# Kernel optimization log

Hardware: AMD Instinct MI355X
Metric: run time of the kernel (lower is better)

## Reference

```python
import jax, jax.numpy as jnp
import numpy as np

N_NODES = 50000
D_IN = 256      # input_rep
D_HID = 256     # num_neurons
N_EDGES = 1600000
N_SAMPLES = 100000


def setup_inputs() -> dict:
    key = jax.random.key(0)
    ks = jax.random.split(key, 12)
    x_feature = jax.random.normal(ks[0], (N_NODES, D_IN), dtype=jnp.float32)
    edge_index = jax.random.randint(ks[1], (2, N_EDGES), 0, N_NODES, dtype=jnp.int64)
    samples = jax.random.randint(ks[2], (N_SAMPLES, 2), 0, N_NODES, dtype=jnp.int64)
    s1 = 1.0 / np.sqrt(D_IN)
    s2 = 1.0 / np.sqrt(D_HID)
    W1 = jax.random.uniform(ks[3], (D_IN, D_HID), jnp.float32, -s1, s1)
    b1 = jax.random.uniform(ks[4], (D_HID,), jnp.float32, -s1, s1)
    W2 = jax.random.uniform(ks[5], (D_HID, D_HID), jnp.float32, -s2, s2)
    b2 = jax.random.uniform(ks[6], (D_HID,), jnp.float32, -s2, s2)
    lin1_W = jax.random.uniform(ks[7], (D_IN, D_IN), jnp.float32, -s1, s1)
    lin1_b = jax.random.uniform(ks[8], (D_IN,), jnp.float32, -s1, s1)
    lin2_W = jax.random.uniform(ks[9], (D_IN, 2), jnp.float32, -s1, s1)
    lin2_b = jax.random.uniform(ks[10], (2,), jnp.float32, -s1, s1)
    return {"x_feature": x_feature, "edge_index": edge_index, "samples": samples,
            "W1": W1, "b1": b1, "W2": W2, "b2": b2,
            "lin1_W": lin1_W, "lin1_b": lin1_b, "lin2_W": lin2_W, "lin2_b": lin2_b}


def _gnn_layer(x, src, dst, W, b, n_nodes):
    # sum-aggregate neighbor messages, then linear (standard GCN-style layer)
    agg = jax.ops.segment_sum(x[src], dst, num_segments=n_nodes)  # [N, d]
    return agg @ W + b


def reference(x_feature, edge_index, samples, W1, b1, W2, b2, lin1_W, lin1_b, lin2_W, lin2_b):
    src, dst = edge_index[0], edge_index[1]
    n = x_feature.shape[0]
    # GNN stack (note: its output is discarded in the original forward; kept for faithfulness)
    h = jax.nn.relu(_gnn_layer(x_feature, src, dst, W1, b1, n))
    h = jax.nn.relu(_gnn_layer(h, src, dst, W2, b2, n))
    # fused gather + elementwise multiply over sampled pairs (replaces per-edge Python loop)
    z = x_feature[samples[:, 0]] * x_feature[samples[:, 1]]  # [S, D_IN]
    z = jax.nn.relu(z @ lin1_W + lin1_b)
    return z @ lin2_W + lin2_b  # [S, 2]
```

## Files before the change

kernel.cpp:

```cpp
#include <hip/hip_runtime.h>

typedef __attribute__((ext_vector_type(8))) short bf16x8;
typedef __attribute__((ext_vector_type(4))) float f32x4;

__device__ __forceinline__ unsigned int f2bf(float f) {
    union { float f; unsigned int u; } v; v.f = f;
    unsigned int u = v.u;
    u += 0x7FFFu + ((u >> 16) & 1u);
    return u >> 16;
}

__global__ void pack_w_kernel(const float* __restrict__ W, unsigned short* __restrict__ P) {
    int tid = blockIdx.x * blockDim.x + threadIdx.x;
    if (tid >= 8192) return;
    int kt   = tid >> 10;
    int f    = (tid >> 6) & 15;
    int lane = tid & 63;
    int k0  = kt * 32 + (lane >> 4) * 8;
    int col = f * 16 + (lane & 15);
    bf16x8 v;
    #pragma unroll
    for (int j = 0; j < 8; ++j)
        v[j] = (short)f2bf(W[(k0 + j) * 256 + col]);
    ((bf16x8*)P)[tid] = v;
}

__global__ __launch_bounds__(256, 4)
void fused_kernel(const float* __restrict__ x,
                  const int* __restrict__ samples,
                  const unsigned short* __restrict__ Wp,
                  const float* __restrict__ b1,
                  const float* __restrict__ w2,
                  const float* __restrict__ b2,
                  float* __restrict__ out, int S)
{
    __shared__ unsigned short zt[4][16][264];

    const int tid  = threadIdx.x;
    const int lane = tid & 63;
    const int wave = tid >> 6;
    const int row0 = blockIdx.x * 64 + wave * 16;
    const int cl   = lane & 15;
    const int hi   = lane >> 4;

    int sidx;
    {
        int i    = row0 * 2 + (lane & 31);
        int imax = 2 * S - 1;
        sidx = samples[i < imax ? i : imax];
    }

    #pragma unroll
    for (int rr = 0; rr < 16; rr += 2) {
        int a0 = __shfl(sidx, 2 * rr,     64);
        int b0 = __shfl(sidx, 2 * rr + 1, 64);
        int a1 = __shfl(sidx, 2 * rr + 2, 64);
        int b1i= __shfl(sidx, 2 * rr + 3, 64);
        f32x4 va0 = ((const f32x4*)x)[(size_t)a0 * 64 + lane];
        f32x4 vb0 = ((const f32x4*)x)[(size_t)b0 * 64 + lane];
        f32x4 va1 = ((const f32x4*)x)[(size_t)a1 * 64 + lane];
        f32x4 vb1 = ((const f32x4*)x)[(size_t)b1i * 64 + lane];
        uint2 u0, u1;
        u0.x = f2bf(va0[0] * vb0[0]) | (f2bf(va0[1] * vb0[1]) << 16);
        u0.y = f2bf(va0[2] * vb0[2]) | (f2bf(va0[3] * vb0[3]) << 16);
        u1.x = f2bf(va1[0] * vb1[0]) | (f2bf(va1[1] * vb1[1]) << 16);
        u1.y = f2bf(va1[2] * vb1[2]) | (f2bf(va1[3] * vb1[3]) << 16);
        *(uint2*)&zt[wave][rr][lane * 4]     = u0;
        *(uint2*)&zt[wave][rr + 1][lane * 4] = u1;
    }

    float b1r[16];
    #pragma unroll
    for (int f = 0; f < 16; ++f) b1r[f] = b1[f * 16 + cl];

    f32x4 acc[16];
    #pragma unroll
    for (int f = 0; f < 16; ++f) acc[f] = (f32x4){0.f, 0.f, 0.f, 0.f};

    const bf16x8* wg = (const bf16x8*)Wp;
    for (int kt = 0; kt < 8; ++kt) {
        bf16x8 af = *(const bf16x8*)&zt[wave][cl][kt * 32 + hi * 8];
        const bf16x8* wk = wg + (size_t)kt * 1024 + lane;
        #pragma unroll
        for (int f = 0; f < 16; ++f) {
            bf16x8 bfr = wk[f * 64];
            acc[f] = __builtin_amdgcn_mfma_f32_16x16x32_bf16(af, bfr, acc[f], 0, 0, 0);
        }
    }

    float p0[4] = {0.f, 0.f, 0.f, 0.f};
    float p1[4] = {0.f, 0.f, 0.f, 0.f};
    #pragma unroll
    for (int f = 0; f < 16; ++f) {
        int c = f * 16 + cl;
        float2 lw = ((const float2*)w2)[c];
        #pragma unroll
        for (int q = 0; q < 4; ++q) {
            float h = fmaxf(acc[f][q] + b1r[f], 0.f);
            p0[q] += h * lw.x;
            p1[q] += h * lw.y;
        }
    }
    #pragma unroll
    for (int m = 1; m < 16; m <<= 1) {
        #pragma unroll
        for (int q = 0; q < 4; ++q) {
            p0[q] += __shfl_xor(p0[q], m, 64);
            p1[q] += __shfl_xor(p1[q], m, 64);
        }
    }
    if (cl < 8) {
        int q = cl >> 1, j = cl & 1;
        int r = row0 + hi * 4 + q;
        if (r < S) {
            float v = (j == 0 ? p0[q] : p1[q]) + b2[j];
            out[r * 2 + j] = v;
        }
    }
}

extern "C" void kernel_launch(void* const* d_in, const int* in_sizes, int n_in,
                              void* d_out, int out_size, void* d_ws, size_t ws_size,
                              hipStream_t stream) {
    const float* x       = (const float*)d_in[0];
    const int*   samples = (const int*)d_in[2];
    const float* lin1_W  = (const float*)d_in[7];
    const float* lin1_b  = (const float*)d_in[8];
    const float* lin2_W  = (const float*)d_in[9];
    const float* lin2_b  = (const float*)d_in[10];
    float* out = (float*)d_out;

    unsigned short* Wp = (unsigned short*)d_ws;
    const int S = in_sizes[2] / 2;

    pack_w_kernel<<<32, 256, 0, stream>>>(lin1_W, Wp);

    const int nblk = (S + 63) / 64;
    fused_kernel<<<nblk, 256, 0, stream>>>(x, samples, Wp, lin1_b, lin2_W, lin2_b, out, S);
}
```

Baseline: 63.20 us.

## Restructure GEMM loop to iterate output tiles with prefetched weight fragments

```diff
diff --git a/kernel.cpp b/kernel.cpp
--- a/kernel.cpp
+++ b/kernel.cpp
@@ -13,8 +13,8 @@
 __global__ void pack_w_kernel(const float* __restrict__ W, unsigned short* __restrict__ P) {
     int tid = blockIdx.x * blockDim.x + threadIdx.x;
     if (tid >= 8192) return;
-    int kt   = tid >> 10;
-    int f    = (tid >> 6) & 15;
+    int f    = tid >> 9;
+    int kt   = (tid >> 6) & 7;
     int lane = tid & 63;
     int k0  = kt * 32 + (lane >> 4) * 8;
     int col = f * 16 + (lane & 15);
@@ -51,56 +51,61 @@
     }
 
     #pragma unroll
-    for (int rr = 0; rr < 16; rr += 2) {
-        int a0 = __shfl(sidx, 2 * rr,     64);
-        int b0 = __shfl(sidx, 2 * rr + 1, 64);
-        int a1 = __shfl(sidx, 2 * rr + 2, 64);
-        int b1i= __shfl(sidx, 2 * rr + 3, 64);
-        f32x4 va0 = ((const f32x4*)x)[(size_t)a0 * 64 + lane];
-        f32x4 vb0 = ((const f32x4*)x)[(size_t)b0 * 64 + lane];
-        f32x4 va1 = ((const f32x4*)x)[(size_t)a1 * 64 + lane];
-        f32x4 vb1 = ((const f32x4*)x)[(size_t)b1i * 64 + lane];
-        uint2 u0, u1;
-        u0.x = f2bf(va0[0] * vb0[0]) | (f2bf(va0[1] * vb0[1]) << 16);
-        u0.y = f2bf(va0[2] * vb0[2]) | (f2bf(va0[3] * vb0[3]) << 16);
-        u1.x = f2bf(va1[0] * vb1[0]) | (f2bf(va1[1] * vb1[1]) << 16);
-        u1.y = f2bf(va1[2] * vb1[2]) | (f2bf(va1[3] * vb1[3]) << 16);
-        *(uint2*)&zt[wave][rr][lane * 4]     = u0;
-        *(uint2*)&zt[wave][rr + 1][lane * 4] = u1;
-    }
-
-    float b1r[16];
-    #pragma unroll
-    for (int f = 0; f < 16; ++f) b1r[f] = b1[f * 16 + cl];
-
-    f32x4 acc[16];
-    #pragma unroll
-    for (int f = 0; f < 16; ++f) acc[f] = (f32x4){0.f, 0.f, 0.f, 0.f};
-
-    const bf16x8* wg = (const bf16x8*)Wp;
-    for (int kt = 0; kt < 8; ++kt) {
-        bf16x8 af = *(const bf16x8*)&zt[wave][cl][kt * 32 + hi * 8];
-        const bf16x8* wk = wg + (size_t)kt * 1024 + lane;
+    for (int g = 0; g < 4; ++g) {
+        f32x4 va[4], vb[4];
         #pragma unroll
-        for (int f = 0; f < 16; ++f) {
-            bf16x8 bfr = wk[f * 64];
-            acc[f] = __builtin_amdgcn_mfma_f32_16x16x32_bf16(af, bfr, acc[f], 0, 0, 0);
+        for (int r = 0; r < 4; ++r) {
+            int a = __shfl(sidx, (g * 4 + r) * 2,     64);
+            int b = __shfl(sidx, (g * 4 + r) * 2 + 1, 64);
+            va[r] = ((const f32x4*)x)[(size_t)a * 64 + lane];
+            vb[r] = ((const f32x4*)x)[(size_t)b * 64 + lane];
+        }
+        #pragma unroll
+        for (int r = 0; r < 4; ++r) {
+            uint2 u;
+            u.x = f2bf(va[r][0] * vb[r][0]) | (f2bf(va[r][1] * vb[r][1]) << 16);
+            u.y = f2bf(va[r][2] * vb[r][2]) | (f2bf(va[r][3] * vb[r][3]) << 16);
+            *(uint2*)&zt[wave][g * 4 + r][lane * 4] = u;
         }
     }
 
+    bf16x8 af[8];
+    #pragma unroll
+    for (int kt = 0; kt < 8; ++kt)
+        af[kt] = *(const bf16x8*)&zt[wave][cl][kt * 32 + hi * 8];
+
+    const bf16x8* wg = (const bf16x8*)Wp + lane;
     float p0[4] = {0.f, 0.f, 0.f, 0.f};
     float p1[4] = {0.f, 0.f, 0.f, 0.f};
+
+    bf16x8 bc[8];
+    #pragma unroll
+    for (int kt = 0; kt < 8; ++kt) bc[kt] = wg[kt * 64];
+
     #pragma unroll
     for (int f = 0; f < 16; ++f) {
-        int c = f * 16 + cl;
-        float2 lw = ((const float2*)w2)[c];
+        bf16x8 bn[8];
+        if (f < 15) {
+            #pragma unroll
+            for (int kt = 0; kt < 8; ++kt) bn[kt] = wg[(f + 1) * 512 + kt * 64];
+        }
+        f32x4 a4 = (f32x4){0.f, 0.f, 0.f, 0.f};
+        #pragma unroll
+        for (int kt = 0; kt < 8; ++kt)
+            a4 = __builtin_amdgcn_mfma_f32_16x16x32_bf16(af[kt], bc[kt], a4, 0, 0, 0);
+
+        float  b1v = b1[f * 16 + cl];
+        float2 lw  = ((const float2*)w2)[f * 16 + cl];
         #pragma unroll
         for (int q = 0; q < 4; ++q) {
-            float h = fmaxf(acc[f][q] + b1r[f], 0.f);
+            float h = fmaxf(a4[q] + b1v, 0.f);
             p0[q] += h * lw.x;
             p1[q] += h * lw.y;
         }
+        #pragma unroll
+        for (int kt = 0; kt < 8; ++kt) bc[kt] = bn[kt];
     }
+
     #pragma unroll
     for (int m = 1; m < 16; m <<= 1) {
         #pragma unroll
```

Result: no change. 62.62 us (-0.9%).
